# Kernel tuning notes

Measured on AMD Instinct MI355X. Metric: run time of the kernel, lower is better.

The kernel has to match this reference:

```python
import jax, jax.numpy as jnp
import numpy as np

H_DIM = 1024
MAX_T = 1024
N_HEADS = 16


def setup_inputs() -> dict:
    key = jax.random.key(0)
    ks = jax.random.split(key, 9)
    B, T, C = 4, 1024, H_DIM
    s = 1.0 / np.sqrt(C)
    return {
        "x": jax.random.normal(ks[0], (B, T, C), jnp.float32),
        "Wq": jax.random.normal(ks[1], (C, H_DIM), jnp.float32) * s,
        "bq": jnp.zeros((H_DIM,), jnp.float32),
        "Wk": jax.random.normal(ks[2], (C, H_DIM), jnp.float32) * s,
        "bk": jnp.zeros((H_DIM,), jnp.float32),
        "Wv": jax.random.normal(ks[3], (C, H_DIM), jnp.float32) * s,
        "bv": jnp.zeros((H_DIM,), jnp.float32),
        "Wo": jax.random.normal(ks[4], (H_DIM, H_DIM), jnp.float32) * s,
        "bo": jnp.zeros((H_DIM,), jnp.float32),
    }


def reference(x, Wq, bq, Wk, bk, Wv, bv, Wo, bo):
    B, T, C = x.shape
    N, D = N_HEADS, C // N_HEADS
    # QKV projections -> [B, N, T, D]
    def split_heads(y):
        return y.reshape(B, T, N, D).transpose(0, 2, 1, 3)
    q = split_heads(x @ Wq + bq)
    k = split_heads(x @ Wk + bk)
    v = split_heads(x @ Wv + bv)
    # scores [B, N, T, T]
    scores = jnp.einsum("bntd,bnsd->bnts", q, k) / jnp.sqrt(jnp.float32(D))
    # Faithful to source: -1e9 added on the LOWER-triangular positions
    mask = jnp.tril(jnp.ones((T, T), jnp.float32)) * (-1e9)
    scores = scores + mask[None, None, :, :]
    attn = jax.nn.softmax(scores, axis=-1)
    out = jnp.einsum("bnts,bnsd->bntd", attn, v)  # [B, N, T, D]
    out = out.transpose(0, 2, 1, 3).reshape(B, T, N * D)
    return out @ Wo + bo
```

## Files before the change

kernel.cpp:

```cpp
#include <hip/hip_runtime.h>
#include <hip/hip_bf16.h>
#include <stdint.h>

#define T_SEQ 1024
#define C_DIM 1024
#define NH 16
#define DH 64

typedef __attribute__((ext_vector_type(8))) __bf16 bf16x8;
typedef __attribute__((ext_vector_type(8))) uint16_t u16x8;
typedef __attribute__((ext_vector_type(4))) float f32x4;

__device__ __forceinline__ uint16_t f2bf(float f) {
    union { float f; uint32_t u; } v; v.f = f;
    uint32_t u = v.u;
    return (uint16_t)((u + 0x7FFFu + ((u >> 16) & 1u)) >> 16);
}
__device__ __forceinline__ float bf2f(uint16_t b) {
    union { uint32_t u; float f; } v; v.u = ((uint32_t)b) << 16; return v.f;
}

__global__ void k_cast(const float* __restrict__ in, uint16_t* __restrict__ out, int n4) {
    int i = blockIdx.x * blockDim.x + threadIdx.x;
    int st = gridDim.x * blockDim.x;
    for (; i < n4; i += st) {
        float4 v = reinterpret_cast<const float4*>(in)[i];
        ushort4 o;
        o.x = f2bf(v.x); o.y = f2bf(v.y); o.z = f2bf(v.z); o.w = f2bf(v.w);
        reinterpret_cast<ushort4*>(out)[i] = o;
    }
}

__global__ void k_transpose4(const float* __restrict__ W0, const float* __restrict__ W1,
                             const float* __restrict__ W2, const float* __restrict__ W3,
                             uint16_t* __restrict__ out) {
    __shared__ float tile[32][33];
    const float* in = (blockIdx.z == 0) ? W0 : (blockIdx.z == 1) ? W1 : (blockIdx.z == 2) ? W2 : W3;
    uint16_t* o = out + ((size_t)blockIdx.z << 20);
    int bx = blockIdx.x * 32;
    int by = blockIdx.y * 32;
    int tx = threadIdx.x, ty = threadIdx.y;
#pragma unroll
    for (int i = 0; i < 4; i++)
        tile[ty + i * 8][tx] = in[(size_t)(by + ty + i * 8) * C_DIM + bx + tx];
    __syncthreads();
#pragma unroll
    for (int i = 0; i < 4; i++)
        o[(size_t)(bx + ty + i * 8) * C_DIM + by + tx] = f2bf(tile[tx][ty + i * 8]);
}

__global__ void k_vmean(const uint16_t* __restrict__ Vt, float* __restrict__ Vmean) {
    const int bh = blockIdx.x;
    const int tid = threadIdx.x;
    const int d = tid >> 2, part = tid & 3;
    const uint16_t* src = Vt + ((size_t)bh * DH + d) * T_SEQ + part * 256;
    float s = 0.f;
#pragma unroll
    for (int i = 0; i < 32; i++) {
        u16x8 v = *reinterpret_cast<const u16x8*>(src + i * 8);
#pragma unroll
        for (int j = 0; j < 8; j++) s += bf2f(v[j]);
    }
    s += __shfl_xor(s, 1);
    s += __shfl_xor(s, 2);
    if (part == 0) Vmean[bh * DH + d] = s * (1.0f / 1024.0f);
}

__device__ __forceinline__ void stage_g64(const uint16_t* A, const uint16_t* Bt, int bm, int bn,
                                          int kt, char* la, char* lb, int tid) {
    const int w = tid >> 6;
#pragma unroll
    for (int i = 0; i < 4; i++) {
        const int r = i * 32 + (tid >> 3);
        const int sc = (((tid & 7) ^ (r & 7))) * 8;
        const uint16_t* ga = A + (size_t)(bm + r) * C_DIM + kt + sc;
        const uint16_t* gb = Bt + (size_t)(bn + r) * C_DIM + kt + sc;
        __builtin_amdgcn_global_load_lds(
            (const __attribute__((address_space(1))) void*)ga,
            (__attribute__((address_space(3))) void*)(la + i * 4096 + w * 1024), 16, 0, 0);
        __builtin_amdgcn_global_load_lds(
            (const __attribute__((address_space(1))) void*)gb,
            (__attribute__((address_space(3))) void*)(lb + i * 4096 + w * 1024), 16, 0, 0);
    }
}

__global__ __launch_bounds__(256) void k_gemm_qkv(const uint16_t* __restrict__ A,
                                                  const uint16_t* __restrict__ Bt,
                                                  const float* __restrict__ bq,
                                                  const float* __restrict__ bk,
                                                  const float* __restrict__ bv,
                                                  uint16_t* __restrict__ qb,
                                                  uint16_t* __restrict__ kb,
                                                  uint16_t* __restrict__ vt) {
    __shared__ uint16_t lA[128 * 64];
    __shared__ uint16_t lB[128 * 64];
    const int bm = blockIdx.x * 128;
    const int bn = blockIdx.y * 128;
    const int tid = threadIdx.x;
    const int lane = tid & 63;
    const int w = tid >> 6;
    const int wm = (w >> 1) * 64;
    const int wn = (w & 1) * 64;
    const int ko = (lane >> 4) * 8;
    const int rr = lane & 15;
    const int sz = (rr & 7) << 3;

    f32x4 acc[4][4] = {};

    for (int kt = 0; kt < C_DIM; kt += 64) {
        stage_g64(A, Bt, bm, bn, kt, (char*)lA, (char*)lB, tid);
        __syncthreads();
#pragma unroll
        for (int kk = 0; kk < 2; kk++) {
            const int pos = (kk * 32 + ko) ^ sz;
            bf16x8 af[4], bfr[4];
#pragma unroll
            for (int i = 0; i < 4; i++) {
                af[i]  = *reinterpret_cast<const bf16x8*>(&lA[(wm + i * 16 + rr) * 64 + pos]);
                bfr[i] = *reinterpret_cast<const bf16x8*>(&lB[(wn + i * 16 + rr) * 64 + pos]);
            }
#pragma unroll
            for (int mi = 0; mi < 4; mi++)
#pragma unroll
                for (int ni = 0; ni < 4; ni++)
                    acc[mi][ni] = __builtin_amdgcn_mfma_f32_16x16x32_bf16(af[mi], bfr[ni], acc[mi][ni], 0, 0, 0);
        }
        __syncthreads();
    }

    const float* bias; uint16_t* outp; int coff, vmode;
    if (bn < 1024)      { bias = bq; outp = qb; coff = 0;    vmode = 0; }
    else if (bn < 2048) { bias = bk; outp = kb; coff = 1024; vmode = 0; }
    else                { bias = bv; outp = vt; coff = 2048; vmode = 1; }

    const int r0 = (lane >> 4) * 4;
    const int cc = lane & 15;
#pragma unroll
    for (int ni = 0; ni < 4; ni++) {
        const int colg = bn + wn + ni * 16 + cc;
        const int col = colg - coff;
        const float bvv = bias[col];
#pragma unroll
        for (int mi = 0; mi < 4; mi++) {
#pragma unroll
            for (int jj = 0; jj < 4; jj++) {
                const int row = bm + wm + mi * 16 + r0 + jj;
                float v = acc[mi][ni][jj] + bvv;
                if (vmode == 0) {
                    outp[(size_t)row * C_DIM + col] = f2bf(v);
                } else {
                    const int b = row >> 10, t2 = row & 1023;
                    const int h = col >> 6, d = col & 63;
                    outp[((size_t)((b * NH + h) * DH + d) << 10) + t2] = f2bf(v);
                }
            }
        }
    }
}

__global__ __launch_bounds__(256) void k_gemm_o(const uint16_t* __restrict__ A,
                                                const uint16_t* __restrict__ Bt,
                                                const float* __restrict__ bias,
                                                float* __restrict__ Out) {
    __shared__ uint16_t lA[128 * 64];
    __shared__ uint16_t lB[128 * 64];
    const int bm = blockIdx.x * 128;
    const int bn = blockIdx.y * 128;
    const int tid = threadIdx.x;
    const int lane = tid & 63;
    const int w = tid >> 6;
    const int wm = (w >> 1) * 64;
    const int wn = (w & 1) * 64;
    const int ko = (lane >> 4) * 8;
    const int rr = lane & 15;
    const int sz = (rr & 7) << 3;

    f32x4 acc[4][4] = {};

    for (int kt = 0; kt < C_DIM; kt += 64) {
        stage_g64(A, Bt, bm, bn, kt, (char*)lA, (char*)lB, tid);
        __syncthreads();
#pragma unroll
        for (int kk = 0; kk < 2; kk++) {
            const int pos = (kk * 32 + ko) ^ sz;
            bf16x8 af[4], bfr[4];
#pragma unroll
            for (int i = 0; i < 4; i++) {
                af[i]  = *reinterpret_cast<const bf16x8*>(&lA[(wm + i * 16 + rr) * 64 + pos]);
                bfr[i] = *reinterpret_cast<const bf16x8*>(&lB[(wn + i * 16 + rr) * 64 + pos]);
            }
#pragma unroll
            for (int mi = 0; mi < 4; mi++)
#pragma unroll
                for (int ni = 0; ni < 4; ni++)
                    acc[mi][ni] = __builtin_amdgcn_mfma_f32_16x16x32_bf16(af[mi], bfr[ni], acc[mi][ni], 0, 0, 0);
        }
        __syncthreads();
    }

    const int r0 = (lane >> 4) * 4;
    const int cc = lane & 15;
#pragma unroll
    for (int ni = 0; ni < 4; ni++) {
        const int col = bn + wn + ni * 16 + cc;
        const float bvv = bias[col];
#pragma unroll
        for (int mi = 0; mi < 4; mi++)
#pragma unroll
            for (int jj = 0; jj < 4; jj++) {
                const int row = bm + wm + mi * 16 + r0 + jj;
                Out[(size_t)row * C_DIM + col] = acc[mi][ni][jj] + bvv;
            }
    }
}

__global__ __launch_bounds__(256, 3) void k_attn(const uint16_t* __restrict__ Q,
                                                 const uint16_t* __restrict__ Kb,
                                                 const uint16_t* __restrict__ Vt,
                                                 const float* __restrict__ Vmean,
                                                 uint16_t* __restrict__ Ob) {
    __shared__ char smem[32768 + 4 * 4608];
    const int tid = threadIdx.x;
    const int lane = tid & 63;
    const int w = tid >> 6;
    uint16_t* lpLo = reinterpret_cast<uint16_t*>(smem + 32768 + w * 4608);
    uint16_t* lpHi = lpLo + 1152;

    const int id = blockIdx.x;
    const int bh = id & 63;
    const int braw = id >> 6;
    const int b = (braw < 4) ? braw : 11 - braw;
    const int q0 = b * 128;
    const int bb = bh >> 4, h = bh & 15;
    const int qq = lane & 15;
    const int gg = lane >> 4;
    const int ko = gg * 8;
    const int r0 = gg * 4;
    const int qgLo = q0 + w * 32 + qq;
    const int qgHi = qgLo + 16;

    const uint16_t* qpLo = Q + (size_t)(bb * T_SEQ + qgLo) * C_DIM + h * DH + ko;
    const uint16_t* qpHi = Q + (size_t)(bb * T_SEQ + qgHi) * C_DIM + h * DH + ko;
    bf16x8 bqLo0 = *reinterpret_cast<const bf16x8*>(qpLo);
    bf16x8 bqLo1 = *reinterpret_cast<const bf16x8*>(qpLo + 32);
    bf16x8 bqHi0 = *reinterpret_cast<const bf16x8*>(qpHi);
    bf16x8 bqHi1 = *reinterpret_cast<const bf16x8*>(qpHi + 32);

    const uint16_t* kbase = Kb + (size_t)bb * T_SEQ * C_DIM + h * DH;
    const uint16_t* vbase = Vt + (size_t)bh * DH * T_SEQ;
    const uint16_t* KL = reinterpret_cast<const uint16_t*>(smem);
    const uint16_t* VL = reinterpret_cast<const uint16_t*>(smem + 16384);

    f32x4 oLo[4] = {}, oHi[4] = {};
    float llLo = 0.f, llHi = 0.f;
    const float zs = 0.125f * 1.44269504088896f;

    const int sz = (qq & 7) << 3;

    const int t0 = b;
    for (int t = t0; t < 8; t++) {
        const int s0 = t * 128;
#pragma unroll
        for (int i = 0; i < 4; i++) {
            const int r = i * 32 + (tid >> 3);
            const int sc = ((tid & 7) ^ (r & 7)) * 8;
            const uint16_t* ks = kbase + (size_t)(s0 + r) * C_DIM + sc;
            __builtin_amdgcn_global_load_lds(
                (const __attribute__((address_space(1))) void*)ks,
                (__attribute__((address_space(3))) void*)(smem + i * 4096 + w * 1024), 16, 0, 0);
        }
#pragma unroll
        for (int i = 0; i < 4; i++) {
            const int r = i * 16 + (tid >> 4);
            const int sc = ((tid & 15) ^ (r & 7)) * 8;
            const uint16_t* vs = vbase + (size_t)r * T_SEQ + s0 + sc;
            __builtin_amdgcn_global_load_lds(
                (const __attribute__((address_space(1))) void*)vs,
                (__attribute__((address_space(3))) void*)(smem + 16384 + i * 4096 + w * 1024), 16, 0, 0);
        }
        __syncthreads();

        uint32_t* lpLo32 = reinterpret_cast<uint32_t*>(lpLo);
        uint32_t* lpHi32 = reinterpret_cast<uint32_t*>(lpHi);
#pragma unroll
        for (int h2 = 0; h2 < 2; h2++) {
#pragma unroll
            for (int hf = 0; hf < 4; hf++) {
                const int rr = h2 * 64 + hf * 16 + qq;
                bf16x8 kf0 = *reinterpret_cast<const bf16x8*>(&KL[rr * 64 + (ko ^ sz)]);
                bf16x8 kf1 = *reinterpret_cast<const bf16x8*>(&KL[rr * 64 + ((32 + ko) ^ sz)]);
                f32x4 sLo = {}, sHi = {};
                sLo = __builtin_amdgcn_mfma_f32_16x16x32_bf16(kf0, bqLo0, sLo, 0, 0, 0);
                sLo = __builtin_amdgcn_mfma_f32_16x16x32_bf16(kf1, bqLo1, sLo, 0, 0, 0);
                sHi = __builtin_amdgcn_mfma_f32_16x16x32_bf16(kf0, bqHi0, sHi, 0, 0, 0);
                sHi = __builtin_amdgcn_mfma_f32_16x16x32_bf16(kf1, bqHi1, sHi, 0, 0, 0);
#pragma unroll
                for (int j = 0; j < 4; j++) {
                    const int k = s0 + h2 * 64 + hf * 16 + r0 + j;
                    const float zLo = sLo[j] * zs + ((k <= qgLo) ? -1e9f : 0.0f);
                    const float zHi = sHi[j] * zs + ((k <= qgHi) ? -1e9f : 0.0f);
                    const float pLo = __builtin_amdgcn_exp2f(zLo);
                    const float pHi = __builtin_amdgcn_exp2f(zHi);
                    sLo[j] = pLo; llLo += pLo;
                    sHi[j] = pHi; llHi += pHi;
                }
#pragma unroll
                for (int jp = 0; jp < 2; jp++) {
                    union { __hip_bfloat162 h2u; uint32_t u; } cL, cH;
                    cL.h2u = __float22bfloat162_rn(make_float2(sLo[2 * jp], sLo[2 * jp + 1]));
                    cH.h2u = __float22bfloat162_rn(make_float2(sHi[2 * jp], sHi[2 * jp + 1]));
                    lpLo32[qq * 36 + hf * 8 + (r0 >> 1) + jp] = cL.u;
                    lpHi32[qq * 36 + hf * 8 + (r0 >> 1) + jp] = cH.u;
                }
            }
            bf16x8 paLo0 = *reinterpret_cast<const bf16x8*>(&lpLo[qq * 72 + ko]);
            bf16x8 paLo1 = *reinterpret_cast<const bf16x8*>(&lpLo[qq * 72 + 32 + ko]);
            bf16x8 paHi0 = *reinterpret_cast<const bf16x8*>(&lpHi[qq * 72 + ko]);
            bf16x8 paHi1 = *reinterpret_cast<const bf16x8*>(&lpHi[qq * 72 + 32 + ko]);
#pragma unroll
            for (int ni = 0; ni < 4; ni++) {
                const int rr = ni * 16 + qq;
                bf16x8 vf0 = *reinterpret_cast<const bf16x8*>(&VL[rr * 128 + ((h2 * 64 + ko) ^ sz)]);
                bf16x8 vf1 = *reinterpret_cast<const bf16x8*>(&VL[rr * 128 + ((h2 * 64 + 32 + ko) ^ sz)]);
                oLo[ni] = __builtin_amdgcn_mfma_f32_16x16x32_bf16(paLo0, vf0, oLo[ni], 0, 0, 0);
                oLo[ni] = __builtin_amdgcn_mfma_f32_16x16x32_bf16(paLo1, vf1, oLo[ni], 0, 0, 0);
                oHi[ni] = __builtin_amdgcn_mfma_f32_16x16x32_bf16(paHi0, vf0, oHi[ni], 0, 0, 0);
                oHi[ni] = __builtin_amdgcn_mfma_f32_16x16x32_bf16(paHi1, vf1, oHi[ni], 0, 0, 0);
            }
        }
        __syncthreads();
    }

    llLo += __shfl_xor(llLo, 16); llLo += __shfl_xor(llLo, 32);
    llHi += __shfl_xor(llHi, 16); llHi += __shfl_xor(llHi, 32);
#pragma unroll
    for (int j = 0; j < 4; j++) {
        {
            const float lr = __shfl(llLo, r0 + j);
            const size_t row = (size_t)(bb * T_SEQ + q0 + w * 32 + r0 + j);
            if (lr > 0.f) {
                const float rinv = 1.0f / lr;
#pragma unroll
                for (int ni = 0; ni < 4; ni++)
                    Ob[row * C_DIM + h * DH + ni * 16 + qq] = f2bf(oLo[ni][j] * rinv);
            } else {
#pragma unroll
                for (int ni = 0; ni < 4; ni++)
                    Ob[row * C_DIM + h * DH + ni * 16 + qq] = f2bf(Vmean[bh * DH + ni * 16 + qq]);
            }
        }
        {
            const float lr = __shfl(llHi, r0 + j);
            const size_t row = (size_t)(bb * T_SEQ + q0 + w * 32 + 16 + r0 + j);
            if (lr > 0.f) {
                const float rinv = 1.0f / lr;
#pragma unroll
                for (int ni = 0; ni < 4; ni++)
                    Ob[row * C_DIM + h * DH + ni * 16 + qq] = f2bf(oHi[ni][j] * rinv);
            } else {
#pragma unroll
                for (int ni = 0; ni < 4; ni++)
                    Ob[row * C_DIM + h * DH + ni * 16 + qq] = f2bf(Vmean[bh * DH + ni * 16 + qq]);
            }
        }
    }
}

extern "C" void kernel_launch(void* const* d_in, const int* in_sizes, int n_in,
                              void* d_out, int out_size, void* d_ws, size_t ws_size,
                              hipStream_t stream) {
    const float* x  = (const float*)d_in[0];
    const float* Wq = (const float*)d_in[1];
    const float* bq = (const float*)d_in[2];
    const float* Wk = (const float*)d_in[3];
    const float* bk = (const float*)d_in[4];
    const float* Wv = (const float*)d_in[5];
    const float* bv = (const float*)d_in[6];
    const float* Wo = (const float*)d_in[7];
    const float* bo = (const float*)d_in[8];
    float* out = (float*)d_out;

    char* ws = (char*)d_ws;
    uint16_t* xb    = (uint16_t*)(ws);
    uint16_t* wqkvt = (uint16_t*)(ws + (8u  << 20));
    float*    vmean = (float*)   (ws + (12u << 20));
    uint16_t* qb    = (uint16_t*)(ws + (16u << 20));
    uint16_t* kb    = (uint16_t*)(ws + (24u << 20));
    uint16_t* vt    = (uint16_t*)(ws + (32u << 20));
    uint16_t* wot   = wqkvt + (3u << 20);
    uint16_t* ab    = qb;

    k_cast<<<2048, 256, 0, stream>>>(x, xb, (4096 * 1024) / 4);
    k_transpose4<<<dim3(32, 32, 4), dim3(32, 8), 0, stream>>>(Wq, Wk, Wv, Wo, wqkvt);

    k_gemm_qkv<<<dim3(32, 24), 256, 0, stream>>>(xb, wqkvt, bq, bk, bv, qb, kb, vt);
    k_vmean<<<64, 256, 0, stream>>>(vt, vmean);
    k_attn<<<512, 256, 0, stream>>>(qb, kb, vt, vmean, ab);
    k_gemm_o<<<dim3(32, 8), 256, 0, stream>>>(ab, wot, bo, out);
}
```

Before: 118.4 us.

## Merge cast and transpose into one prep kernel; shrink GEMM K-tile to 32

The x cast and the four weight transposes now run in a single launch, with the block index choosing the role, which saves one kernel launch and the gap between launches. Both GEMMs also stage K in chunks of 32 instead of 64, halving shared memory per block with a new XOR swizzle for the narrower rows. This can raise occupancy, but it doubles the number of loop iterations and barrier pairs per output tile.

```diff
diff --git a/kernel.cpp b/kernel.cpp
--- a/kernel.cpp
+++ b/kernel.cpp
@@ -20,26 +20,31 @@
     union { uint32_t u; float f; } v; v.u = ((uint32_t)b) << 16; return v.f;
 }
 
-__global__ void k_cast(const float* __restrict__ in, uint16_t* __restrict__ out, int n4) {
-    int i = blockIdx.x * blockDim.x + threadIdx.x;
-    int st = gridDim.x * blockDim.x;
-    for (; i < n4; i += st) {
-        float4 v = reinterpret_cast<const float4*>(in)[i];
-        ushort4 o;
-        o.x = f2bf(v.x); o.y = f2bf(v.y); o.z = f2bf(v.z); o.w = f2bf(v.w);
-        reinterpret_cast<ushort4*>(out)[i] = o;
-    }
-}
-
-__global__ void k_transpose4(const float* __restrict__ W0, const float* __restrict__ W1,
-                             const float* __restrict__ W2, const float* __restrict__ W3,
-                             uint16_t* __restrict__ out) {
+__global__ void k_prep(const float* __restrict__ x,
+                       const float* __restrict__ W0, const float* __restrict__ W1,
+                       const float* __restrict__ W2, const float* __restrict__ W3,
+                       uint16_t* __restrict__ xb, uint16_t* __restrict__ wout) {
+    const int gid = blockIdx.x;
+    if (gid < 2048) {
+        int i = gid * 256 + threadIdx.x;
+        const int st = 2048 * 256;
+#pragma unroll
+        for (int it = 0; it < 2; it++, i += st) {
+            float4 v = reinterpret_cast<const float4*>(x)[i];
+            ushort4 o;
+            o.x = f2bf(v.x); o.y = f2bf(v.y); o.z = f2bf(v.z); o.w = f2bf(v.w);
+            reinterpret_cast<ushort4*>(xb)[i] = o;
+        }
+        return;
+    }
     __shared__ float tile[32][33];
-    const float* in = (blockIdx.z == 0) ? W0 : (blockIdx.z == 1) ? W1 : (blockIdx.z == 2) ? W2 : W3;
-    uint16_t* o = out + ((size_t)blockIdx.z << 20);
-    int bx = blockIdx.x * 32;
-    int by = blockIdx.y * 32;
-    int tx = threadIdx.x, ty = threadIdx.y;
+    const int id2 = gid - 2048;
+    const int z = id2 >> 10;
+    const int by = ((id2 >> 5) & 31) * 32;
+    const int bx = (id2 & 31) * 32;
+    const float* in = (z == 0) ? W0 : (z == 1) ? W1 : (z == 2) ? W2 : W3;
+    uint16_t* o = wout + ((size_t)z << 20);
+    const int tx = threadIdx.x & 31, ty = threadIdx.x >> 5;
 #pragma unroll
     for (int i = 0; i < 4; i++)
         tile[ty + i * 8][tx] = in[(size_t)(by + ty + i * 8) * C_DIM + bx + tx];
@@ -66,21 +71,20 @@
     if (part == 0) Vmean[bh * DH + d] = s * (1.0f / 1024.0f);
 }
 
-__device__ __forceinline__ void stage_g64(const uint16_t* A, const uint16_t* Bt, int bm, int bn,
-                                          int kt, char* la, char* lb, int tid) {
-    const int w = tid >> 6;
-#pragma unroll
-    for (int i = 0; i < 4; i++) {
-        const int r = i * 32 + (tid >> 3);
-        const int sc = (((tid & 7) ^ (r & 7))) * 8;
-        const uint16_t* ga = A + (size_t)(bm + r) * C_DIM + kt + sc;
-        const uint16_t* gb = Bt + (size_t)(bn + r) * C_DIM + kt + sc;
+__device__ __forceinline__ void stage_g(const uint16_t* A, const uint16_t* Bt, int bm, int bn,
+                                        int kt, char* la, char* lb, int tid) {
+    const int w = tid >> 6, srow = tid >> 2;
+    const int scol = (((tid & 3) ^ ((srow >> 1) & 3))) * 8;
+#pragma unroll
+    for (int p = 0; p < 2; p++) {
+        const uint16_t* ga = A + (size_t)(bm + p * 64 + srow) * C_DIM + kt + scol;
+        const uint16_t* gb = Bt + (size_t)(bn + p * 64 + srow) * C_DIM + kt + scol;
         __builtin_amdgcn_global_load_lds(
             (const __attribute__((address_space(1))) void*)ga,
-            (__attribute__((address_space(3))) void*)(la + i * 4096 + w * 1024), 16, 0, 0);
+            (__attribute__((address_space(3))) void*)(la + p * 4096 + w * 1024), 16, 0, 0);
         __builtin_amdgcn_global_load_lds(
             (const __attribute__((address_space(1))) void*)gb,
-            (__attribute__((address_space(3))) void*)(lb + i * 4096 + w * 1024), 16, 0, 0);
+            (__attribute__((address_space(3))) void*)(lb + p * 4096 + w * 1024), 16, 0, 0);
     }
 }
 
@@ -92,8 +96,8 @@
                                                   uint16_t* __restrict__ qb,
                                                   uint16_t* __restrict__ kb,
                                                   uint16_t* __restrict__ vt) {
-    __shared__ uint16_t lA[128 * 64];
-    __shared__ uint16_t lB[128 * 64];
+    __shared__ uint16_t lA[128 * 32];
+    __shared__ uint16_t lB[128 * 32];
     const int bm = blockIdx.x * 128;
     const int bn = blockIdx.y * 128;
     const int tid = threadIdx.x;
@@ -103,28 +107,24 @@
     const int wn = (w & 1) * 64;
     const int ko = (lane >> 4) * 8;
     const int rr = lane & 15;
-    const int sz = (rr & 7) << 3;
+    const int pos = ko ^ (((rr >> 1) & 3) << 3);
 
     f32x4 acc[4][4] = {};
 
-    for (int kt = 0; kt < C_DIM; kt += 64) {
-        stage_g64(A, Bt, bm, bn, kt, (char*)lA, (char*)lB, tid);
-        __syncthreads();
-#pragma unroll
-        for (int kk = 0; kk < 2; kk++) {
-            const int pos = (kk * 32 + ko) ^ sz;
-            bf16x8 af[4], bfr[4];
-#pragma unroll
-            for (int i = 0; i < 4; i++) {
-                af[i]  = *reinterpret_cast<const bf16x8*>(&lA[(wm + i * 16 + rr) * 64 + pos]);
-                bfr[i] = *reinterpret_cast<const bf16x8*>(&lB[(wn + i * 16 + rr) * 64 + pos]);
-            }
-#pragma unroll
-            for (int mi = 0; mi < 4; mi++)
-#pragma unroll
-                for (int ni = 0; ni < 4; ni++)
-                    acc[mi][ni] = __builtin_amdgcn_mfma_f32_16x16x32_bf16(af[mi], bfr[ni], acc[mi][ni], 0, 0, 0);
-        }
+    for (int kt = 0; kt < C_DIM; kt += 32) {
+        stage_g(A, Bt, bm, bn, kt, (char*)lA, (char*)lB, tid);
+        __syncthreads();
+        bf16x8 af[4], bfr[4];
+#pragma unroll
+        for (int i = 0; i < 4; i++) {
+            af[i]  = *reinterpret_cast<const bf16x8*>(&lA[(wm + i * 16 + rr) * 32 + pos]);
+            bfr[i] = *reinterpret_cast<const bf16x8*>(&lB[(wn + i * 16 + rr) * 32 + pos]);
+        }
+#pragma unroll
+        for (int mi = 0; mi < 4; mi++)
+#pragma unroll
+            for (int ni = 0; ni < 4; ni++)
+                acc[mi][ni] = __builtin_amdgcn_mfma_f32_16x16x32_bf16(af[mi], bfr[ni], acc[mi][ni], 0, 0, 0);
         __syncthreads();
     }
 
@@ -162,8 +162,8 @@
                                                 const uint16_t* __restrict__ Bt,
                                                 const float* __restrict__ bias,
                                                 float* __restrict__ Out) {
-    __shared__ uint16_t lA[128 * 64];
-    __shared__ uint16_t lB[128 * 64];
+    __shared__ uint16_t lA[128 * 32];
+    __shared__ uint16_t lB[128 * 32];
     const int bm = blockIdx.x * 128;
     const int bn = blockIdx.y * 128;
     const int tid = threadIdx.x;
@@ -173,28 +173,24 @@
     const int wn = (w & 1) * 64;
     const int ko = (lane >> 4) * 8;
     const int rr = lane & 15;
-    const int sz = (rr & 7) << 3;
+    const int pos = ko ^ (((rr >> 1) & 3) << 3);
 
     f32x4 acc[4][4] = {};
 
-    for (int kt = 0; kt < C_DIM; kt += 64) {
-        stage_g64(A, Bt, bm, bn, kt, (char*)lA, (char*)lB, tid);
-        __syncthreads();
-#pragma unroll
-        for (int kk = 0; kk < 2; kk++) {
-            const int pos = (kk * 32 + ko) ^ sz;
-            bf16x8 af[4], bfr[4];
-#pragma unroll
-            for (int i = 0; i < 4; i++) {
-                af[i]  = *reinterpret_cast<const bf16x8*>(&lA[(wm + i * 16 + rr) * 64 + pos]);
-                bfr[i] = *reinterpret_cast<const bf16x8*>(&lB[(wn + i * 16 + rr) * 64 + pos]);
-            }
-#pragma unroll
-            for (int mi = 0; mi < 4; mi++)
-#pragma unroll
-                for (int ni = 0; ni < 4; ni++)
-                    acc[mi][ni] = __builtin_amdgcn_mfma_f32_16x16x32_bf16(af[mi], bfr[ni], acc[mi][ni], 0, 0, 0);
-        }
+    for (int kt = 0; kt < C_DIM; kt += 32) {
+        stage_g(A, Bt, bm, bn, kt, (char*)lA, (char*)lB, tid);
+        __syncthreads();
+        bf16x8 af[4], bfr[4];
+#pragma unroll
+        for (int i = 0; i < 4; i++) {
+            af[i]  = *reinterpret_cast<const bf16x8*>(&lA[(wm + i * 16 + rr) * 32 + pos]);
+            bfr[i] = *reinterpret_cast<const bf16x8*>(&lB[(wn + i * 16 + rr) * 32 + pos]);
+        }
+#pragma unroll
+        for (int mi = 0; mi < 4; mi++)
+#pragma unroll
+            for (int ni = 0; ni < 4; ni++)
+                acc[mi][ni] = __builtin_amdgcn_mfma_f32_16x16x32_bf16(af[mi], bfr[ni], acc[mi][ni], 0, 0, 0);
         __syncthreads();
     }
 
@@ -390,8 +386,7 @@
     uint16_t* wot   = wqkvt + (3u << 20);
     uint16_t* ab    = qb;
 
-    k_cast<<<2048, 256, 0, stream>>>(x, xb, (4096 * 1024) / 4);
-    k_transpose4<<<dim3(32, 32, 4), dim3(32, 8), 0, stream>>>(Wq, Wk, Wv, Wo, wqkvt);
+    k_prep<<<6144, 256, 0, stream>>>(x, Wq, Wk, Wv, Wo, xb, wqkvt);
 
     k_gemm_qkv<<<dim3(32, 24), 256, 0, stream>>>(xb, wqkvt, bq, bk, bv, qb, kb, vt);
     k_vmean<<<64, 256, 0, stream>>>(vt, vmean);
```

Result: faster. 103.2 us (-12.8%).
